# Optimization experiments

Hardware: AMD Instinct MI355X
Metric: run time of the kernel (lower is better)

## Reference

```python
import jax, jax.numpy as jnp
import numpy as np

# ---- p4m group tables (g = 4*m + r, m in {0,1} mirror, r in {0..3} rot90) ----
def _p4m_tables():
    R = np.array([[0, -1], [1, 0]])
    F = np.array([[-1, 0], [0, 1]])
    I = np.eye(2, dtype=int)
    mats = []
    for m in (0, 1):
        for r in range(4):
            mats.append(np.linalg.matrix_power(R, r) @ (F if m else I))
    def idx(M):
        for i, A in enumerate(mats):
            if np.array_equal(A, M):
                return i
        raise ValueError('not in group')
    comp = np.array([[idx(mats[a] @ mats[b]) for b in range(8)] for a in range(8)])
    inv = np.array([idx(mats[a].T) for a in range(8)])  # orthogonal -> inv = transpose
    return comp, inv

COMP, INV = _p4m_tables()

def _transform_kernel(g, W):
    # L_g applied to filter spatial axes: mirror (last axis) then rotate r times
    m, r = g // 4, g % 4
    if m:
        W = jnp.flip(W, axis=-1)
    return jnp.rot90(W, k=r, axes=(-2, -1))

STRIDE, PADDING, DILATION = 1, 1, 1

def setup_inputs() -> dict:
    key = jax.random.key(0)
    k1, k2 = jax.random.split(key)
    B, Cin, Cout, H, W, kH, kW = 16, 64, 64, 64, 64, 3, 3
    x = jax.random.normal(k1, (B, Cin, 8, H, W), dtype=jnp.float32)
    scale = 1.0 / np.sqrt(Cin * kH * kW)
    weight_rel = jax.random.normal(k2, (Cout, Cin, 8, kH, kW), dtype=jnp.float32) * scale
    bias = jnp.zeros((Cout,), dtype=jnp.float32)
    return {'x': x, 'weight_rel': weight_rel, 'bias': bias}

def _gconv(x, weight_rel, bias):
    B, Cin, N, H, Wd = x.shape  # N == 8
    Cout, _, _, kH, kW = weight_rel.shape
    # Build the full group-equivariant filter bank once (fused form of the
    # original 64 small conv2d calls): bank[g*Cout+co, c*8+h] = L_g psi(g^{-1} h)
    banks = []
    for g in range(8):
        u = COMP[INV[g]]                # [8] relative element u = g^{-1} h, for h=0..7
        Wg = weight_rel[:, :, u]        # [Cout, Cin, 8, kH, kW]
        banks.append(_transform_kernel(g, Wg))
    bank = jnp.stack(banks, 0)          # [8, Cout, Cin, 8, kH, kW]
    bank = bank.reshape(8 * Cout, Cin * 8, kH, kW)
    x2 = x.reshape(B, Cin * 8, H, Wd)   # in-channel index = c*8 + h, matches bank
    y = jax.lax.conv_general_dilated(
        x2, bank,
        window_strides=(STRIDE, STRIDE),
        padding=[(PADDING, PADDING), (PADDING, PADDING)],
        rhs_dilation=(DILATION, DILATION),
        dimension_numbers=('NCHW', 'OIHW', 'NCHW'))
    Ho, Wo = y.shape[-2], y.shape[-1]
    y = y.reshape(B, 8, Cout, Ho, Wo).transpose(0, 2, 1, 3, 4)  # [B, Cout, 8, Ho, Wo]
    return y + bias[None, :, None, None, None]

def reference(x, weight_rel, bias):
    return _gconv(x, weight_rel, bias)
```

## Files before the change

### kernel.cpp

```cpp
#include <hip/hip_runtime.h>
#include <stdint.h>

typedef short  bf16x8 __attribute__((ext_vector_type(8)));
typedef float  f32x4  __attribute__((ext_vector_type(4)));


__device__ __forceinline__ short f2bf(float f) {
    uint32_t u = __builtin_bit_cast(uint32_t, f);
    u += 0x7FFFu + ((u >> 16) & 1u);
    return (short)(u >> 16);
}

__device__ __forceinline__ int u_index(int g, int s) {
    int r  = g & 3, m  = g >> 2;
    int r2 = s & 3, ms = s >> 2;
    if (!m) { int rr = (r2 - r) & 3; return ms ? (4 + rr) : rr; }
    else    { int rr = (r - r2) & 3; return ms ? rr : (4 + rr); }
}

__device__ __forceinline__ void gload_lds16(const void* g, void* l) {
    __builtin_amdgcn_global_load_lds(
        (const __attribute__((address_space(1))) uint32_t*)g,
        (__attribute__((address_space(3))) uint32_t*)l, 16, 0, 0);
}

#define XB_BYTES  (16LL * 66 * 66 * 512 * 2)
#define BK_BYTES  (16LL * 9 * 4 * 512 * 8 * 2)
#define WS_NEEDED (XB_BYTES + BK_BYTES)


__global__ __launch_bounds__(256) void prep_x2(const float* __restrict__ x,
                                               short* __restrict__ xb) {
    __shared__ float t[64][65];
    const int h = blockIdx.x, kc8 = blockIdx.y, b = blockIdx.z;
    const int k0 = kc8 * 64;
    const int tid = threadIdx.x;
    const int w  = tid & 63, kq = tid >> 6;
    const float* xp = x + ((size_t)(b * 512 + k0 + kq) * 4096) + h * 64 + w;
    #pragma unroll
    for (int i = 0; i < 16; ++i)
        t[kq + 4 * i][w] = xp[(size_t)(4 * i) * 4096];
    __syncthreads();
    const int w2 = tid >> 3, kk = tid & 7;
    #pragma unroll
    for (int half = 0; half < 2; ++half) {
        const int ww = w2 + 32 * half;
        bf16x8 v;
        #pragma unroll
        for (int j = 0; j < 8; ++j) v[j] = f2bf(t[kk * 8 + j][ww]);
        size_t o = (((size_t)b * 66 + h + 1) * 66 + (ww + 1)) * 512 + k0 + kk * 8;
        *reinterpret_cast<bf16x8*>(&xb[o]) = v;
    }
}

__global__ __launch_bounds__(256) void zero_border(short* __restrict__ xb) {
    int idx = blockIdx.x * 256 + threadIdx.x;
    if (idx >= 16 * 260 * 64) return;
    int kg = idx & 63;
    int rest = idx >> 6;
    int b  = rest / 260;
    int pe = rest - b * 260;
    int hh, ww;
    if      (pe < 66)  { hh = 0;            ww = pe; }
    else if (pe < 132) { hh = 65;           ww = pe - 66; }
    else if (pe < 196) { hh = pe - 132 + 1; ww = 0; }
    else               { hh = pe - 196 + 1; ww = 65; }
    size_t o = (((size_t)b * 66 + hh) * 66 + ww) * 512 + kg * 8;
    bf16x8 z = {0,0,0,0,0,0,0,0};
    *reinterpret_cast<bf16x8*>(&xb[o]) = z;
}

__global__ __launch_bounds__(256) void prep_w(const float* __restrict__ wrel,
                                              short* __restrict__ bank) {
    int tg = blockIdx.x * 256 + threadIdx.x;
    int oc = tg & 511;
    int kg = (tg >> 9) & 3;
    int kc = (tg >> 11) & 15;
    int t  = tg >> 15;
    int ki = t / 3, kj = t - ki * 3;
    int g = oc & 7, co = oc >> 3;
    int r = g & 3, m = g >> 2;
    int a0, b0;
    switch (r) {
        case 0:  a0 = ki;     b0 = kj;     break;
        case 1:  a0 = kj;     b0 = 2 - ki; break;
        case 2:  a0 = 2 - ki; b0 = 2 - kj; break;
        default: a0 = 2 - kj; b0 = ki;     break;
    }
    if (m) b0 = 2 - b0;
    int ci = kc * 4 + kg;
    const float* wp = wrel + (size_t)(co * 64 + ci) * 72 + a0 * 3 + b0;
    bf16x8 v;
    #pragma unroll
    for (int j = 0; j < 8; ++j) v[j] = f2bf(wp[u_index(g, j) * 9]);
    size_t o = ((((size_t)kc * 9 + t) * 4 + kg) * 512 + oc) * 8;
    *reinterpret_cast<bf16x8*>(&bank[o]) = v;
}

#define XS_SLOTS 39
#define XS_SH    (XS_SLOTS * 512)
#define WS_SH    (36 * 512)

#define STAGE(XS, WS, kc)                                                  \
    {                                                                      \
        _Pragma("unroll")                                                  \
        for (int q = 0; q < 9; ++q) {                                      \
            int it = wid + 4 * q;                                          \
            gload_lds16(bank + (size_t)(kc) * 147456 + woff[q],            \
                        &WS[it * 512]);                                    \
        }                                                                  \
        _Pragma("unroll")                                                  \
        for (int q = 0; q < 10; ++q) {                                     \
            int it = wid + 4 * q;                                          \
            if (it < XS_SLOTS)                                             \
                gload_lds16(xb + (size_t)xoff[q] + (kc) * 32,              \
                            &XS[it * 512]);                                \
        }                                                                  \
    }

#define COMPUTE(XS, WS)                                                    \
    {                                                                      \
        _Pragma("unroll")                                                  \
        for (int kj = 0; kj < 3; ++kj) {                                   \
            bf16x8 bfr[6][2];                                              \
            _Pragma("unroll")                                              \
            for (int rr = 0; rr < 6; ++rr)                                 \
                _Pragma("unroll")                                          \
                for (int cg = 0; cg < 2; ++cg)                             \
                    bfr[rr][cg] = *reinterpret_cast<const bf16x8*>(        \
                        &XS[(lkg * 624 + (wid * 4 + rr) * 34               \
                             + cg * 16 + l15 + kj) * 8]);                  \
            _Pragma("unroll")                                              \
            for (int ki = 0; ki < 3; ++ki) {                               \
                const int t = ki * 3 + kj;                                 \
                bf16x8 a[4];                                               \
                _Pragma("unroll")                                          \
                for (int mi = 0; mi < 4; ++mi)                             \
                    a[mi] = *reinterpret_cast<const bf16x8*>(              \
                        &WS[((t * 4 + lkg) * 64 + mi * 16 + l15) * 8]);    \
                _Pragma("unroll")                                          \
                for (int nj = 0; nj < 8; ++nj) {                           \
                    bf16x8 bv = bfr[(nj & 3) + ki][nj >> 2];               \
                    _Pragma("unroll")                                      \
                    for (int mi = 0; mi < 4; ++mi)                         \
                        acc[mi][nj] =                                      \
                            __builtin_amdgcn_mfma_f32_16x16x32_bf16(       \
                                a[mi], bv, acc[mi][nj], 0, 0, 0);          \
                }                                                          \
            }                                                              \
        }                                                                  \
    }

__global__ __launch_bounds__(256, 1) void gconv_mfma(
    const short* __restrict__ xb, const short* __restrict__ bank,
    const float* __restrict__ bias, float* __restrict__ out)
{
    __shared__ __attribute__((aligned(16))) short xsA[XS_SH], xsB[XS_SH];
    __shared__ __attribute__((aligned(16))) short wsA[WS_SH], wsB[WS_SH];

    const int st  = blockIdx.x;
    const int ot  = blockIdx.y;
    const int b   = blockIdx.z;
    const int h0  = (st >> 1) * 16;
    const int w0  = (st & 1) * 32;
    const int oc0 = ot * 64;

    const int tid  = threadIdx.x;
    const int lane = tid & 63;
    const int wid  = tid >> 6;
    const int l15  = lane & 15;
    const int lkg  = lane >> 4;

    f32x4 acc[4][8];
    #pragma unroll
    for (int i = 0; i < 4; ++i)
        #pragma unroll
        for (int j = 0; j < 8; ++j)
            #pragma unroll
            for (int e = 0; e < 4; ++e) acc[i][j][e] = 0.f;

    const int xrow_base = (b * 66 + h0) * 66 + w0;

    int xoff[10];
    #pragma unroll
    for (int q = 0; q < 10; ++q) {
        int it = wid + 4 * q;
        if (it >= XS_SLOTS) it = XS_SLOTS - 1;
        int slot = it * 64 + lane;
        int kg = slot / 624;
        int px = slot - kg * 624;
        px = px < 612 ? px : 611;
        int r = px / 34;
        int c = px - r * 34;
        xoff[q] = (xrow_base + r * 66 + c) * 512 + kg * 8;
    }
    int woff[9];
    #pragma unroll
    for (int q = 0; q < 9; ++q) {
        int it = wid + 4 * q;
        int t  = it >> 2, kg = it & 3;
        woff[q] = ((t * 4 + kg) * 512 + oc0 + lane) * 8;
    }

    STAGE(xsA, wsA, 0);
    __syncthreads();
    for (int kc2 = 0; kc2 < 8; ++kc2) {
        STAGE(xsB, wsB, 2 * kc2 + 1);
        COMPUTE(xsA, wsA);
        __syncthreads();
        if (kc2 < 7) STAGE(xsA, wsA, 2 * kc2 + 2);
        COMPUTE(xsB, wsB);
        __syncthreads();
    }

    #pragma unroll
    for (int mi = 0; mi < 4; ++mi) {
        #pragma unroll
        for (int j = 0; j < 4; ++j) {
            const int oc_g = oc0 + mi * 16 + lkg * 4 + j;
            const float bv = bias[oc_g >> 3];
            float* op = out + ((size_t)b * 512 + oc_g) * 4096;
            #pragma unroll
            for (int nj = 0; nj < 8; ++nj) {
                const int hh = h0 + wid * 4 + (nj & 3);
                const int wwp = w0 + (nj >> 2) * 16 + l15;
                op[hh * 64 + wwp] = acc[mi][nj][j] + bv;
            }
        }
    }
}

__global__ __launch_bounds__(256) void gconv_direct(
    const float* __restrict__ x, const float* __restrict__ wrel,
    const float* __restrict__ bias, float* __restrict__ out)
{
    __shared__ float xsf[18][20];
    __shared__ float wsf[16][9];
    const int st = blockIdx.x, ct = blockIdx.y, b = blockIdx.z;
    const int h0 = (st >> 2) * 16, w0 = (st & 3) * 16, oc0 = ct * 16;
    const int tid = threadIdx.x;
    const int ch = tid & 15, blk = tid >> 4;
    const int by = (blk >> 2) * 4, bx = (blk & 3) * 4;
    const int oc = oc0 + ch, g = oc & 7, co = oc >> 3;
    const int wl_c = tid / 9, wl_k = tid - wl_c * 9;
    const int wl_i = wl_k / 3, wl_j = wl_k - wl_i * 3;
    const int wl_oc = oc0 + wl_c, wl_g = wl_oc & 7, wl_co = wl_oc >> 3;
    int a0, b0;
    { const int r = wl_g & 3, m = wl_g >> 2;
      switch (r) { case 0: a0=wl_i; b0=wl_j; break; case 1: a0=wl_j; b0=2-wl_i; break;
                   case 2: a0=2-wl_i; b0=2-wl_j; break; default: a0=2-wl_j; b0=wl_i; break; }
      if (m) b0 = 2 - b0; }
    float acc[4][4];
    #pragma unroll
    for (int i=0;i<4;++i) for (int j=0;j<4;++j) acc[i][j]=0.f;
    for (int t = 0; t < 512; ++t) {
        const int ci = t >> 3, s = t & 7;
        __syncthreads();
        const float* xp = x + (((size_t)(b * 64 + ci) * 8 + s) * 4096);
        for (int idx = tid; idx < 18 * 18; idx += 256) {
            const int rr = idx / 18, cc = idx - rr * 18;
            const int gh = h0 - 1 + rr, gw = w0 - 1 + cc;
            float v = 0.f;
            if (gh >= 0 && gh < 64 && gw >= 0 && gw < 64) v = xp[gh * 64 + gw];
            xsf[rr][cc] = v;
        }
        if (tid < 144) {
            const int u = u_index(wl_g, s);
            wsf[wl_c][wl_k] = wrel[((size_t)(wl_co*64+ci)*8+u)*9 + a0*3 + b0];
        }
        __syncthreads();
        float wr[9];
        #pragma unroll
        for (int k=0;k<9;++k) wr[k]=wsf[ch][k];
        float xv[6][6];
        #pragma unroll
        for (int i=0;i<6;++i) for (int j=0;j<6;++j) xv[i][j]=xsf[by+i][bx+j];
        #pragma unroll
        for (int py=0;py<4;++py) for (int px=0;px<4;++px)
            for (int ki=0;ki<3;++ki) for (int kj=0;kj<3;++kj)
                acc[py][px] += xv[py+ki][px+kj]*wr[ki*3+kj];
    }
    const float bv = bias[co];
    float* op = out + (((size_t)(b*64+co)*8+g)*4096);
    #pragma unroll
    for (int py=0;py<4;++py) for (int px=0;px<4;++px)
        op[(h0+by+py)*64 + (w0+bx+px)] = acc[py][px] + bv;
}

extern "C" void kernel_launch(void* const* d_in, const int* in_sizes, int n_in,
                              void* d_out, int out_size, void* d_ws, size_t ws_size,
                              hipStream_t stream) {
    const float* x    = (const float*)d_in[0];
    const float* wrel = (const float*)d_in[1];
    const float* bias = (const float*)d_in[2];
    float* out        = (float*)d_out;

    if (ws_size >= (size_t)WS_NEEDED) {
        short* xb   = (short*)d_ws;
        short* bank = (short*)((char*)d_ws + XB_BYTES);
        zero_border<<<1040, 256, 0, stream>>>(xb);
        {
            dim3 g(64, 8, 16);
            prep_x2<<<g, 256, 0, stream>>>(x, xb);
        }
        prep_w<<<1152, 256, 0, stream>>>(wrel, bank);
        dim3 grid(8, 8, 16);
        gconv_mfma<<<grid, 256, 0, stream>>>(xb, bank, bias, out);
    } else {
        dim3 grid(16, 32, 16);
        gconv_direct<<<grid, 256, 0, stream>>>(x, wrel, bias, out);
    }
}
```

Before: 328.1 us.

## Widen MFMA block to 128 output channels with 8 waves sharing input tile

Each block now has 512 threads (8 waves) and covers 128 output channels instead of 64. The same staged input tile serves both 64-channel halves, which halves global-to-LDS traffic for the input per output. The weight buffer grows to cover 128 channels but is now single-buffered. Weight loads are therefore issued between compute phases behind extra barriers and are no longer overlapped with MFMA work. The launch bound of 512 threads with 2 blocks per CU, together with the 128-float accumulator per thread, risks register spills, and LDS use of about 150 KB may allow only one block per CU.

```diff
diff --git a/kernel.cpp b/kernel.cpp
--- a/kernel.cpp
+++ b/kernel.cpp
@@ -99,26 +99,30 @@
 
 #define XS_SLOTS 39
 #define XS_SH    (XS_SLOTS * 512)
-#define WS_SH    (36 * 512)
-
-#define STAGE(XS, WS, kc)                                                  \
+#define WS_SH    (72 * 512)
+
+#define STAGE_X(XS, kc)                                                    \
     {                                                                      \
         _Pragma("unroll")                                                  \
-        for (int q = 0; q < 9; ++q) {                                      \
-            int it = wid + 4 * q;                                          \
-            gload_lds16(bank + (size_t)(kc) * 147456 + woff[q],            \
-                        &WS[it * 512]);                                    \
-        }                                                                  \
-        _Pragma("unroll")                                                  \
-        for (int q = 0; q < 10; ++q) {                                     \
-            int it = wid + 4 * q;                                          \
+        for (int q = 0; q < 5; ++q) {                                      \
+            int it = wid + 8 * q;                                          \
             if (it < XS_SLOTS)                                             \
                 gload_lds16(xb + (size_t)xoff[q] + (kc) * 32,              \
                             &XS[it * 512]);                                \
         }                                                                  \
     }
 
-#define COMPUTE(XS, WS)                                                    \
+#define STAGE_W(kc)                                                        \
+    {                                                                      \
+        _Pragma("unroll")                                                  \
+        for (int q = 0; q < 9; ++q) {                                      \
+            int gq = wid + 8 * q;                               \
+            gload_lds16(bank + (size_t)(kc) * 147456 + woff[q],            \
+                        &wsm[gq * 512]);                                   \
+        }                                                                  \
+    }
+
+#define COMPUTE(XS)                                                        \
     {                                                                      \
         _Pragma("unroll")                                                  \
         for (int kj = 0; kj < 3; ++kj) {                                   \
@@ -128,7 +132,7 @@
                 _Pragma("unroll")                                          \
                 for (int cg = 0; cg < 2; ++cg)                             \
                     bfr[rr][cg] = *reinterpret_cast<const bf16x8*>(        \
-                        &XS[(lkg * 624 + (wid * 4 + rr) * 34               \
+                        &XS[(lkg * 624 + (wp * 4 + rr) * 34                \
                              + cg * 16 + l15 + kj) * 8]);                  \
             _Pragma("unroll")                                              \
             for (int ki = 0; ki < 3; ++ki) {                               \
@@ -137,7 +141,8 @@
                 _Pragma("unroll")                                          \
                 for (int mi = 0; mi < 4; ++mi)                             \
                     a[mi] = *reinterpret_cast<const bf16x8*>(              \
-                        &WS[((t * 4 + lkg) * 64 + mi * 16 + l15) * 8]);    \
+                        &wsm[((t * 4 + lkg) * 128 + wo * 64               \
+                              + mi * 16 + l15) * 8]);                      \
                 _Pragma("unroll")                                          \
                 for (int nj = 0; nj < 8; ++nj) {                           \
                     bf16x8 bv = bfr[(nj & 3) + ki][nj >> 2];               \
@@ -151,23 +156,25 @@
         }                                                                  \
     }
 
-__global__ __launch_bounds__(256, 1) void gconv_mfma(
+__global__ __launch_bounds__(512, 2) void gconv_mfma(
     const short* __restrict__ xb, const short* __restrict__ bank,
     const float* __restrict__ bias, float* __restrict__ out)
 {
     __shared__ __attribute__((aligned(16))) short xsA[XS_SH], xsB[XS_SH];
-    __shared__ __attribute__((aligned(16))) short wsA[WS_SH], wsB[WS_SH];
+    __shared__ __attribute__((aligned(16))) short wsm[WS_SH];
 
     const int st  = blockIdx.x;
     const int ot  = blockIdx.y;
     const int b   = blockIdx.z;
     const int h0  = (st >> 1) * 16;
     const int w0  = (st & 1) * 32;
-    const int oc0 = ot * 64;
+    const int oc0 = ot * 128;
 
     const int tid  = threadIdx.x;
     const int lane = tid & 63;
     const int wid  = tid >> 6;
+    const int wo   = wid >> 2;
+    const int wp   = wid & 3;
     const int l15  = lane & 15;
     const int lkg  = lane >> 4;
 
@@ -181,10 +188,10 @@
 
     const int xrow_base = (b * 66 + h0) * 66 + w0;
 
-    int xoff[10];
-    #pragma unroll
-    for (int q = 0; q < 10; ++q) {
-        int it = wid + 4 * q;
+    int xoff[5];
+    #pragma unroll
+    for (int q = 0; q < 5; ++q) {
+        int it = wid + 8 * q;
         if (it >= XS_SLOTS) it = XS_SLOTS - 1;
         int slot = it * 64 + lane;
         int kg = slot / 624;
@@ -197,32 +204,40 @@
     int woff[9];
     #pragma unroll
     for (int q = 0; q < 9; ++q) {
-        int it = wid + 4 * q;
-        int t  = it >> 2, kg = it & 3;
-        woff[q] = ((t * 4 + kg) * 512 + oc0 + lane) * 8;
-    }
-
-    STAGE(xsA, wsA, 0);
+        int gq  = wid + 8 * q;
+        int tkg = gq >> 1;
+        int och = gq & 1;
+        woff[q] = (tkg * 512 + oc0 + och * 64 + lane) * 8;
+    }
+
+    STAGE_X(xsA, 0);
+    STAGE_W(0);
     __syncthreads();
     for (int kc2 = 0; kc2 < 8; ++kc2) {
-        STAGE(xsB, wsB, 2 * kc2 + 1);
-        COMPUTE(xsA, wsA);
-        __syncthreads();
-        if (kc2 < 7) STAGE(xsA, wsA, 2 * kc2 + 2);
-        COMPUTE(xsB, wsB);
-        __syncthreads();
+        STAGE_X(xsB, 2 * kc2 + 1);
+        COMPUTE(xsA);
+        __syncthreads();
+        STAGE_W(2 * kc2 + 1);
+        __syncthreads();
+        if (kc2 < 7) STAGE_X(xsA, 2 * kc2 + 2);
+        COMPUTE(xsB);
+        __syncthreads();
+        if (kc2 < 7) {
+            STAGE_W(2 * kc2 + 2);
+            __syncthreads();
+        }
     }
 
     #pragma unroll
     for (int mi = 0; mi < 4; ++mi) {
         #pragma unroll
         for (int j = 0; j < 4; ++j) {
-            const int oc_g = oc0 + mi * 16 + lkg * 4 + j;
+            const int oc_g = oc0 + wo * 64 + mi * 16 + lkg * 4 + j;
             const float bv = bias[oc_g >> 3];
             float* op = out + ((size_t)b * 512 + oc_g) * 4096;
             #pragma unroll
             for (int nj = 0; nj < 8; ++nj) {
-                const int hh = h0 + wid * 4 + (nj & 3);
+                const int hh = h0 + wp * 4 + (nj & 3);
                 const int wwp = w0 + (nj >> 2) * 16 + l15;
                 op[hh * 64 + wwp] = acc[mi][nj][j] + bv;
             }
@@ -304,8 +319,8 @@
             prep_x2<<<g, 256, 0, stream>>>(x, xb);
         }
         prep_w<<<1152, 256, 0, stream>>>(wrel, bank);
-        dim3 grid(8, 8, 16);
-        gconv_mfma<<<grid, 256, 0, stream>>>(xb, bank, bias, out);
+        dim3 grid(8, 4, 16);
+        gconv_mfma<<<grid, 512, 0, stream>>>(xb, bank, bias, out);
     } else {
         dim3 grid(16, 32, 16);
         gconv_direct<<<grid, 256, 0, stream>>>(x, wrel, bias, out);
```

Result: slower. 405.2 us (median of 4 runs) (+23.5%).
